# Kernel optimization log

Hardware: AMD Instinct MI355X
Metric: run time of the kernel (lower is better)

## Reference

```python
import jax, jax.numpy as jnp
import numpy as np
import math

# ---- module config (mirrors init_kwargs) ----
FRAME_H, FRAME_W = 480, 640
HFOV = 79.0
CAM_H_CM = 88.0            # camera_height * 100
NUM_SEM = 16
RES = 5                    # map_resolution (cm/cell)
MAP_SIZE_CM = 4800
DSC = 4                    # global_downscaling
DU = 4                     # du_scale
VR = 100                   # vision_range (cells)
CAT_THR, EXP_THR, MAP_THR = 5.0, 1.0, 1.0
MIN_D_CM, MAX_D_CM = 50.0, 350.0
NC = 6                     # MC.NON_SEM_CHANNELS
ML = MAP_SIZE_CM // DSC // RES   # 240 local map cells
MG = MAP_SIZE_CM // RES          # 960 global map cells
ZMIN = int(-40 / RES)            # -8
ZB = int(360 / RES) - ZMIN       # 80 z bins
MIN_MAP_H = int(25 / RES - ZMIN)            # 13
MAX_MAP_H = int((CAM_H_CM + 1) / RES - ZMIN)  # 25
BC_R = 200 // RES                # been-close radius (cells)
CENTER_POSE = (ML * RES) / 200.0 # agent start at local map center (m)


def _affine_grid(theta, H, W):
    # theta: (B,2,3); align_corners=True convention
    ys = jnp.linspace(-1.0, 1.0, H)
    xs = jnp.linspace(-1.0, 1.0, W)
    xg, yg = jnp.meshgrid(xs, ys)
    base = jnp.stack([xg, yg, jnp.ones_like(xg)], -1)  # (H,W,3)
    return jnp.einsum('bij,hwj->bhwi', theta, base)    # (B,H,W,2)


def _grid_sample(img, grid):
    # bilinear, align_corners=True, zero padding (matches F.grid_sample)
    B, C, H, W = img.shape
    x = (grid[..., 0] + 1.0) * 0.5 * (W - 1)
    y = (grid[..., 1] + 1.0) * 0.5 * (H - 1)
    x0, y0 = jnp.floor(x), jnp.floor(y)
    flat = img.reshape(B, C, H * W)
    out = jnp.zeros_like(img)
    for dx in (0.0, 1.0):
        for dy in (0.0, 1.0):
            xi, yi = x0 + dx, y0 + dy
            w = (1.0 - jnp.abs(x - xi)) * (1.0 - jnp.abs(y - yi))
            ok = (xi >= 0) & (xi <= W - 1) & (yi >= 0) & (yi <= H - 1)
            idx = (jnp.clip(yi, 0, H - 1).astype(jnp.int32) * W
                   + jnp.clip(xi, 0, W - 1).astype(jnp.int32))
            g = jnp.take_along_axis(flat, jnp.broadcast_to(idx.reshape(B, 1, -1), (B, C, H * W)), axis=2)
            out = out + g.reshape(B, C, H, W) * (w * ok)[:, None]
    return out


def _splat(gx, gy, gz, feat, valid):
    # trilinear scatter-add of per-point features into (VR,VR,ZB) voxel grid
    # gx,gy,gz,valid: (B,P); feat: (B,P,F)
    B, P = gx.shape
    F = feat.shape[-1]
    ncell = VR * VR * ZB
    acc = jnp.zeros((B * ncell, F), feat.dtype)
    base = (jnp.arange(B) * ncell)[:, None]
    x0, y0, z0 = jnp.floor(gx), jnp.floor(gy), jnp.floor(gz)
    for dx in (0.0, 1.0):
        for dy in (0.0, 1.0):
            for dz in (0.0, 1.0):
                xi, yi, zi = x0 + dx, y0 + dy, z0 + dz
                w = (1.0 - jnp.abs(gx - xi)) * (1.0 - jnp.abs(gy - yi)) * (1.0 - jnp.abs(gz - zi))
                ok = valid & (xi >= 0) & (xi < VR) & (yi >= 0) & (yi < VR) & (zi >= 0) & (zi < ZB)
                cell = (yi.astype(jnp.int32) * VR + xi.astype(jnp.int32)) * ZB + zi.astype(jnp.int32)
                idx = jnp.clip(base + cell, 0, B * ncell - 1).reshape(-1)
                upd = (feat * (w * ok.astype(feat.dtype))[..., None]).reshape(B * P, F)
                acc = acc.at[idx].add(upd)
    return acc.reshape(B, VR, VR, ZB, F).transpose(0, 4, 1, 2, 3)  # (B,F,VR,VR,ZB)


def _forward(seq_obs, seq_pose_delta, seq_camera_poses, init_local_map,
             init_global_map, init_local_pose, init_global_pose,
             init_lmb, init_origins, seq_dones, seq_update_global):
    B, T = seq_obs.shape[:2]
    C = NUM_SEM
    f = FRAME_W / (2.0 * math.tan(math.radians(HFOV) / 2.0))
    cx, cy = FRAME_W / 2.0, FRAME_H / 2.0
    xs = ((jnp.arange(0, FRAME_W, DU) - cx) / f).astype(jnp.float32)   # (Ws,)
    zr = ((cy - jnp.arange(0, FRAME_H, DU)) / f).astype(jnp.float32)   # (Hs,)
    # camera tilt (elevation) from extrinsics (identity -> 0)
    elev = jnp.arctan2(seq_camera_poses[:, 2, 1], seq_camera_poses[:, 2, 2])
    ce, se = jnp.cos(elev)[:, None, None], jnp.sin(elev)[:, None, None]
    Hs, Ws = FRAME_H // DU, FRAME_W // DU
    P = Hs * Ws
    row = jnp.arange(ML, dtype=jnp.float32)

    def step(carry, inp):
        local_map, global_map, pose = carry
        obs, pd, done, upd = inp
        done = done.astype(bool)
        upd = upd.astype(bool)
        # episode reset
        local_map = jnp.where(done[:, None, None, None], 0.0, local_map)
        global_map = jnp.where(done[:, None, None, None], 0.0, global_map)
        pose = jnp.where(done[:, None], jnp.array([CENTER_POSE, CENTER_POSE, 0.0], jnp.float32), pose)
        # pose update (get_new_pose_batch, degrees)
        tr = jnp.radians(pose[:, 2])
        nx = pose[:, 0] + pd[:, 0] * jnp.cos(tr) - pd[:, 1] * jnp.sin(tr)
        ny = pose[:, 1] + pd[:, 0] * jnp.sin(tr) + pd[:, 1] * jnp.cos(tr)
        nt = jnp.mod(pose[:, 2] + jnp.degrees(pd[:, 2]) + 180.0, 360.0) - 180.0
        pose = jnp.stack([nx, ny, nt], -1)
        # ---- depth -> egocentric point cloud (cm) ----
        d = obs[:, 3, ::DU, ::DU]                           # (B,Hs,Ws)
        valid = (d >= MIN_D_CM) & (d <= MAX_D_CM)
        lat = d * xs[None, None, :]
        up = d * zr[None, :, None]
        fwd = d * ce + up * se
        hgt = -d * se + up * ce + CAM_H_CM
        gx = (lat / RES + VR / 2.0).reshape(B, P)
        gy = (fwd / RES).reshape(B, P)
        gz = (hgt / RES - ZMIN).reshape(B, P)
        # features: occupancy + avg-pooled semantics (du_scale pooling)
        sem = obs[:, 4:].reshape(B, C, Hs, DU, Ws, DU).mean((3, 5))
        feat = jnp.concatenate([jnp.ones((B, 1, Hs, Ws), obs.dtype), sem], 1)
        feat = feat.reshape(B, 1 + C, P).transpose(0, 2, 1)  # (B,P,F)
        vox = _splat(gx, gy, gz, feat, valid.reshape(B, P))  # (B,F,VR,VR,ZB)
        agent_hp = vox[..., MIN_MAP_H:MAX_MAP_H].sum(-1)
        all_hp = vox.sum(-1)
        fp_map = jnp.clip(agent_hp[:, 0:1] / MAP_THR, 0.0, 1.0)
        fp_exp = jnp.clip(all_hp[:, 0:1] / EXP_THR, 0.0, 1.0)
        sem_pred = jnp.clip(agent_hp[:, 1:] / CAT_THR, 0.0, 1.0)
        agent_view = jnp.zeros((B, NC + C, ML, ML), obs.dtype)
        y1, x1 = ML // 2, ML // 2 - VR // 2
        agent_view = agent_view.at[:, 0:1, y1:y1 + VR, x1:x1 + VR].set(fp_map)
        agent_view = agent_view.at[:, 1:2, y1:y1 + VR, x1:x1 + VR].set(fp_exp)
        agent_view = agent_view.at[:, NC:, y1:y1 + VR, x1:x1 + VR].set(sem_pred)
        # ---- pose transform: rotation then translation grid_sample ----
        th = jnp.radians(90.0 - pose[:, 2])
        stx = -(pose[:, 0] * 100.0 / RES - ML / 2.0) / (ML / 2.0)
        sty = -(pose[:, 1] * 100.0 / RES - ML / 2.0) / (ML / 2.0)
        c, s = jnp.cos(th), jnp.sin(th)
        z0 = jnp.zeros_like(th)
        o1 = jnp.ones_like(th)
        th_rot = jnp.stack([jnp.stack([c, -s, z0], -1), jnp.stack([s, c, z0], -1)], 1)
        th_tr = jnp.stack([jnp.stack([o1, z0, stx], -1), jnp.stack([z0, o1, sty], -1)], 1)
        warped = _grid_sample(_grid_sample(agent_view, _affine_grid(th_rot, ML, ML)),
                              _affine_grid(th_tr, ML, ML))
        # dilate obstacle channel (3x3 ones kernel, 1 iter)
        obst = jax.lax.reduce_window(warped[:, 0:1], -jnp.inf, jax.lax.max,
                                     (1, 1, 3, 3), (1, 1, 1, 1), 'SAME')
        warped = warped.at[:, 0:1].set(obst)
        local_map = jnp.maximum(local_map, warped)
        # current location / visited / been-close disks
        acx, acy = pose[:, 0] * 100.0 / RES, pose[:, 1] * 100.0 / RES
        d2 = ((row[None, None, :] - acx[:, None, None]) ** 2
              + (row[None, :, None] - acy[:, None, None]) ** 2)
        curr = (d2 <= 4.0).astype(local_map.dtype)
        local_map = local_map.at[:, 2].set(curr)
        local_map = local_map.at[:, 3].max(curr)
        local_map = local_map.at[:, 4].max((d2 <= float(BC_R ** 2)).astype(local_map.dtype))
        # global map update at local map boundaries
        gnew = jax.vmap(lambda g, l, lm: jax.lax.dynamic_update_slice(g, l, (0, lm[0], lm[2])))(
            global_map, local_map, init_lmb)
        global_map = jnp.where(upd[:, None, None, None], gnew, global_map)
        gpose = pose + init_origins
        # map features: local NC ch + maxpooled global NC ch + local sem ch
        gmax = global_map[:, :NC].reshape(B, NC, MG // DSC, DSC, MG // DSC, DSC).max((3, 5))
        mf = jnp.concatenate([local_map[:, :NC], gmax, local_map[:, NC:]], 1)
        return (local_map, global_map, pose), (mf, pose, gpose)

    xs_t = (jnp.swapaxes(seq_obs, 0, 1), jnp.swapaxes(seq_pose_delta, 0, 1),
            jnp.swapaxes(seq_dones, 0, 1), jnp.swapaxes(seq_update_global, 0, 1))
    (fl, fg, _), (mfs, lps, gps) = jax.lax.scan(
        step, (init_local_map, init_global_map, init_local_pose), xs_t)
    seq_mf = jnp.swapaxes(mfs, 0, 1)
    seq_lp = jnp.swapaxes(lps, 0, 1)
    seq_gp = jnp.swapaxes(gps, 0, 1)
    seq_lmb = jnp.broadcast_to(init_lmb[:, None], (B, T, 4))
    seq_org = jnp.broadcast_to(init_origins[:, None], (B, T, 3))
    return seq_mf, fl, fg, seq_lp, seq_gp, seq_lmb, seq_org


def setup_inputs():
    key = jax.random.key(0)
    k0, k1 = jax.random.split(key)
    B, T = 4, 4
    obs = jax.random.uniform(k0, (B, T, 4 + NUM_SEM, FRAME_H, FRAME_W), jnp.float32)
    obs = obs.at[:, :, 3].set(MIN_D_CM + obs[:, :, 3] * (MAX_D_CM - MIN_D_CM))  # depth in cm
    obs = obs.at[:, :, 4:].set((obs[:, :, 4:] > 0.9).astype(jnp.float32))       # binary seg masks
    pd = jax.random.normal(k1, (B, T, 3), jnp.float32) * jnp.array([0.25, 0.05, 0.1], jnp.float32)
    lo = (MG - ML) // 2
    lmb = jnp.tile(jnp.array([[lo, lo + ML, lo, lo + ML]], jnp.int32), (B, 1))
    origins = jnp.concatenate([jnp.full((B, 2), lo * RES / 100.0, jnp.float32),
                               jnp.zeros((B, 1), jnp.float32)], 1)
    lp = jnp.concatenate([jnp.full((B, 2), CENTER_POSE, jnp.float32),
                          jnp.zeros((B, 1), jnp.float32)], 1)
    return {
        "seq_obs": obs,
        "seq_pose_delta": pd,
        "seq_camera_poses": jnp.broadcast_to(jnp.eye(4, dtype=jnp.float32), (B, 4, 4)),
        "init_local_map": jnp.zeros((B, NC + NUM_SEM, ML, ML), jnp.float32),
        "init_global_map": jnp.zeros((B, NC + NUM_SEM, MG, MG), jnp.float32),
        "init_local_pose": lp,
        "init_global_pose": lp + origins,
        "init_origins": origins,
        "seq_dones": jnp.zeros((B, T), jnp.int32),
        "seq_update_global": jnp.ones((B, T), jnp.int32),
        "init_lmb": lmb,
    }


def reference(seq_obs, seq_pose_delta, seq_camera_poses, init_local_map, init_global_map,
              init_local_pose, init_global_pose, init_origins, seq_dones,
              seq_update_global, init_lmb):
    return _forward(seq_obs, seq_pose_delta, seq_camera_poses, init_local_map,
                    init_global_map, init_local_pose, init_global_pose,
                    init_lmb, init_origins, seq_dones, seq_update_global)
```

## Files before the change

### kernel.cpp

```cpp
#include <hip/hip_runtime.h>
#include <math.h>

#ifndef M_PI
#define M_PI 3.14159265358979323846
#endif

#define BB 4
#define TT 4
#define NSEM 16
#define CHL 22
#define CHMF 28
#define ML 240
#define MG 960
#define VR 100
#define HS 120
#define WSW 160
#define NPL 18
#define CPAD 24
#define MLSQ (ML*ML)
#define MGSQ (MG*MG)
#define VRSQ (VR*VR)
#define PPT (HS*WSW)
#define NPART 12
#define PR 9
#define NGRP 5

#define SZ_MF (BB*TT*CHMF*MLSQ)
#define SZ_FL (BB*CHL*MLSQ)
#define SZ_FG (BB*CHL*MGSQ)
#define OFF_FL SZ_MF
#define OFF_FG (OFF_FL + SZ_FL)
#define OFF_LP (OFF_FG + SZ_FG)
#define OFF_GP (OFF_LP + BB*TT*3)
#define OFF_LMB (OFF_GP + BB*TT*3)
#define OFF_ORG (OFF_LMB + BB*TT*4)

#define WS_SCAL 0
#define WS_FLAGS (WS_SCAL + BB*TT*8)
#define WS_CACHE (WS_FLAGS + 4*BB)
#define WS_PLANES (WS_CACHE + BB*6*MLSQ)
#define WS_I2 (WS_PLANES + BB*TT*VRSQ*CPAD)
#define PTSN (BB*TT*PPT)
#define WS_GY (WS_I2 + BB*TT*NPL*MLSQ)
#define WS_GX (WS_GY + PTSN)
#define WS_WZA (WS_GX + PTSN)
#define WS_WZL (WS_WZA + PTSN)
#define WS_SEMDS (WS_WZL + PTSN)

__global__ __launch_bounds__(256) void k_stage1(const float* __restrict__ obs,
                                                const float* __restrict__ cam,
                                                const float* __restrict__ pd,
                                                const float* __restrict__ ilp,
                                                const float* __restrict__ org,
                                                const int* __restrict__ lmb,
                                                const int* __restrict__ dones,
                                                const int* __restrict__ updg,
                                                float* __restrict__ out,
                                                float* __restrict__ ws)
{
    if (blockIdx.x == 0) {
        int i = threadIdx.x;
        if (i < BB*TT) {
            int b = i / TT, t = i % TT;
            for (int k = 0; k < 4; k++) out[OFF_LMB + (b*TT+t)*4 + k] = (float)lmb[b*4+k];
            for (int k = 0; k < 3; k++) out[OFF_ORG + (b*TT+t)*3 + k] = org[b*3+k];
        }
        if (i >= BB) return;
        int b = i;
        float p0 = ilp[b*3+0], p1 = ilp[b*3+1], p2 = ilp[b*3+2];
        const float D2R = 0.017453292519943295f;
        int lastDone = -1, lastUpd = -1;
        for (int t = 0; t < TT; t++) {
            if (dones[b*TT+t]) { p0 = 6.0f; p1 = 6.0f; p2 = 0.0f; lastDone = t; }
            if (updg[b*TT+t]) lastUpd = t;
            float tr = p2 * D2R;
            float c0 = cosf(tr), s0 = sinf(tr);
            float q0 = pd[(b*TT+t)*3+0], q1 = pd[(b*TT+t)*3+1], q2 = pd[(b*TT+t)*3+2];
            float nx = p0 + q0*c0 - q1*s0;
            float ny = p1 + q0*s0 + q1*c0;
            float a  = p2 + q2*57.29577951308232f + 180.0f;
            float m  = fmodf(a, 360.0f); if (m < 0.0f) m += 360.0f;
            float nt = m - 180.0f;
            p0 = nx; p1 = ny; p2 = nt;
            out[OFF_LP + (b*TT+t)*3+0] = nx;
            out[OFF_LP + (b*TT+t)*3+1] = ny;
            out[OFF_LP + (b*TT+t)*3+2] = nt;
            out[OFF_GP + (b*TT+t)*3+0] = nx + org[b*3+0];
            out[OFF_GP + (b*TT+t)*3+1] = ny + org[b*3+1];
            out[OFF_GP + (b*TT+t)*3+2] = nt + org[b*3+2];
            float th = (90.0f - nt) * D2R;
            float ax = nx*100.0f/5.0f, ay = ny*100.0f/5.0f;
            float* sc = ws + WS_SCAL + (b*TT+t)*8;
            sc[0] = cosf(th);
            sc[1] = sinf(th);
            sc[2] = -(ax - 120.0f)/120.0f;
            sc[3] = -(ay - 120.0f)/120.0f;
            sc[4] = ax;
            sc[5] = ay;
        }
        ws[WS_FLAGS + b*4 + 0] = (lastDone >= 0) ? 1.0f : 0.0f;
        ws[WS_FLAGS + b*4 + 1] = (lastUpd < lastDone) ? 1.0f : 0.0f;
        ws[WS_FLAGS + b*4 + 2] = (float)lastUpd;
        return;
    }
    int bb = blockIdx.x - 1;
    int bt = bb / 75;
    int b = bt / TT;
    int p = (bb % 75)*256 + threadIdx.x;
    int h = p / WSW, w = p % WSW;
    size_t pi = (size_t)bt*PPT + p;
    const float* ob = obs + (size_t)bt * 20 * 480 * 640;
    float d = ob[(size_t)(3*480 + 4*h)*640 + 4*w];
    if (!(d >= 50.0f && d <= 350.0f)) { ws[WS_GY + pi] = -1000.0f; return; }

    double fd = 640.0 / (2.0 * tan((79.0 * M_PI / 180.0) * 0.5));
    float ff  = (float)fd;
    float xsv = (float)(4*w - 320) / ff;
    float zrv = (240.0f - (float)(4*h)) / ff;
    float elev = atan2f(cam[b*16+9], cam[b*16+10]);
    float ce = cosf(elev), se = sinf(elev);
    float up  = d * zrv;
    float fwd = d*ce + up*se;
    float hgt = -d*se + up*ce + 88.0f;
    float gx = (d*xsv)/5.0f + 50.0f;
    float gy = fwd/5.0f;
    float gz = hgt/5.0f + 8.0f;

    float z0 = floorf(gz);
    float wza = 0.0f, wzl = 0.0f;
    #pragma unroll
    for (int dz = 0; dz < 2; dz++) {
        float zi = z0 + dz;
        float wz = 1.0f - fabsf(gz - zi);
        if (zi >= 0.0f && zi < 80.0f) {
            wzl += wz;
            if (zi >= 13.0f && zi < 25.0f) wza += wz;
        }
    }
    if (wzl == 0.0f && wza == 0.0f) { ws[WS_GY + pi] = -1000.0f; return; }

    ws[WS_GY + pi]  = gy;
    ws[WS_GX + pi]  = gx;
    ws[WS_WZA + pi] = wza;
    ws[WS_WZL + pi] = wzl;

    if (wza > 0.0f) {
        const float* sb = ob + (size_t)4*480*640 + (size_t)(4*h)*640 + 4*w;
        float* so = ws + WS_SEMDS + (size_t)bt*NSEM*PPT + p;
        #pragma unroll
        for (int k = 0; k < NSEM; k++) {
            float s = 0.0f;
            #pragma unroll
            for (int r = 0; r < 4; r++) {
                const float4 v = *(const float4*)(sb + (size_t)k*480*640 + r*640);
                s += v.x + v.y + v.z + v.w;
            }
            so[(size_t)k*PPT] = s * 0.0625f;
        }
    }
}

__global__ __launch_bounds__(256) void k_splat2(const float* __restrict__ ws,
                                                float* __restrict__ planes)
{
    int bt = blockIdx.x;
    int part = blockIdx.y;
    int grp = blockIdx.z;
    int rlo = part * PR;
    int c0  = (grp == 0) ? 0 : (2 + 4*(grp-1));
    int nch = (grp == 0) ? 2 : 4;
    __shared__ float acc[4*PR*VR];
    for (int e = threadIdx.x; e < nch*PR*VR; e += 256) acc[e] = 0.0f;
    __syncthreads();

    const float* gyA  = ws + WS_GY  + (size_t)bt*PPT;
    const float* gxA  = ws + WS_GX  + (size_t)bt*PPT;
    const float* wzaA = ws + WS_WZA + (size_t)bt*PPT;
    const float* wzlA = ws + WS_WZL + (size_t)bt*PPT;
    const float* semA = ws + WS_SEMDS + (size_t)bt*NSEM*PPT + (size_t)(c0-2)*PPT;

    for (int p = threadIdx.x; p < PPT; p += 256) {
        float gy = gyA[p];
        float y0 = floorf(gy);
        if (y0 > (float)(rlo + PR - 1) || y0 + 1.0f < (float)rlo) continue;
        float wza = wzaA[p];
        if (grp != 0 && wza <= 0.0f) continue;
        float gx  = gxA[p];
        float x0 = floorf(gx);
        float sem[4];
        if (grp != 0) {
            #pragma unroll
            for (int k = 0; k < 4; k++) sem[k] = semA[(size_t)k*PPT + p];
        }
        float wzl = (grp == 0) ? wzlA[p] : 0.0f;
        #pragma unroll
        for (int dy = 0; dy < 2; dy++) {
            float yi = y0 + dy;
            if (!(yi >= 0.0f && yi < 100.0f)) continue;
            int r = (int)yi - rlo;
            if (r < 0 || r >= PR) continue;
            float wy = 1.0f - fabsf(gy - yi);
            #pragma unroll
            for (int dx = 0; dx < 2; dx++) {
                float xi = x0 + dx;
                if (!(xi >= 0.0f && xi < 100.0f)) continue;
                float wxy = (1.0f - fabsf(gx - xi)) * wy;
                if (wxy <= 0.0f) continue;
                int cell = r*VR + (int)xi;
                if (grp == 0) {
                    if (wza > 0.0f) atomicAdd(&acc[cell], wza*wxy);
                    if (wzl > 0.0f) atomicAdd(&acc[PR*VR + cell], wzl*wxy);
                } else {
                    #pragma unroll
                    for (int k = 0; k < 4; k++) {
                        float sv = sem[k];
                        if (sv != 0.0f) atomicAdd(&acc[k*PR*VR + cell], sv*wza*wxy);
                    }
                }
            }
        }
    }
    __syncthreads();

    int nrows = 100 - rlo; if (nrows > PR) nrows = PR;
    if (nrows <= 0) return;
    float* pl = planes + (size_t)bt*VRSQ*CPAD;
    for (int e = threadIdx.x; e < nch*nrows*VR; e += 256) {
        int c = e / (nrows*VR);
        int rc = e % (nrows*VR);
        int r = rc / VR, x = rc % VR;
        pl[(size_t)((rlo + r)*VR + x)*CPAD + (c0 + c)] = acc[c*PR*VR + r*VR + x];
    }
}

__global__ __launch_bounds__(256) void k_stage3(const float* __restrict__ planes,
                                                const float* __restrict__ igm,
                                                const int* __restrict__ dones,
                                                const int* __restrict__ lmb,
                                                float* __restrict__ I2,
                                                float* __restrict__ fg,
                                                float* __restrict__ out,
                                                float* __restrict__ ws)
{
    int bid = blockIdx.x;
    if (bid < 3600) {
        int bt = bid / 225;
        int idx = (bid % 225)*256 + threadIdx.x;
        int i = idx / ML, j = idx % ML;
        const float* sc = ws + WS_SCAL + bt*8;
        float c = sc[0], s = sc[1], stx = sc[2], sty = sc[3];
        float* o = I2 + (size_t)bt*NPL*MLSQ + idx;
        const float* pl = planes + (size_t)bt*VRSQ*CPAD;

        int   soff[16];
        float sw[16];
        float wsum = 0.0f;
        {
            float xg = (float)j * (float)(2.0/239.0) - 1.0f + stx;
            float yg = (float)i * (float)(2.0/239.0) - 1.0f + sty;
            float x = (xg + 1.0f)*0.5f*239.0f;
            float y = (yg + 1.0f)*0.5f*239.0f;
            float x0 = floorf(x), y0 = floorf(y);
            #pragma unroll
            for (int dy = 0; dy < 2; dy++) {
                float yi = y0 + dy;
                bool vy = (yi >= 0.0f && yi <= 239.0f);
                float wy = 1.0f - fabsf(y - yi);
                #pragma unroll
                for (int dx = 0; dx < 2; dx++) {
                    float xi = x0 + dx;
                    bool vx = (xi >= 0.0f && xi <= 239.0f);
                    float w2v = (vy && vx) ? (1.0f - fabsf(x - xi)) * wy : 0.0f;
                    int ci = (dy*2 + dx)*4;
                    float xg1 = (float)(int)xi * (float)(2.0/239.0) - 1.0f;
                    float yg1 = (float)(int)yi * (float)(2.0/239.0) - 1.0f;
                    float gxr = c*xg1 - s*yg1;
                    float gyr = s*xg1 + c*yg1;
                    float xx = (gxr + 1.0f)*0.5f*239.0f;
                    float yy = (gyr + 1.0f)*0.5f*239.0f;
                    float xx0 = floorf(xx), yy0 = floorf(yy);
                    #pragma unroll
                    for (int dy1 = 0; dy1 < 2; dy1++) {
                        float syi = yy0 + dy1;
                        bool v1y = (syi >= 120.0f && syi < 220.0f);
                        float wy1 = 1.0f - fabsf(yy - syi);
                        #pragma unroll
                        for (int dx1 = 0; dx1 < 2; dx1++) {
                            float sxi = xx0 + dx1;
                            bool v1 = v1y && (sxi >= 70.0f && sxi < 170.0f);
                            float w1v = v1 ? (1.0f - fabsf(xx - sxi)) * wy1 : 0.0f;
                            float wt = w2v * w1v;
                            soff[ci + dy1*2 + dx1] = v1 ? ((int)syi - 120)*VR + ((int)sxi - 70) : 0;
                            sw[ci + dy1*2 + dx1] = wt;
                            wsum += wt;
                        }
                    }
                }
            }
        }

        if (wsum <= 0.0f) {
            #pragma unroll
            for (int cc = 0; cc < NPL; cc++) o[(size_t)cc*MLSQ] = 0.0f;
            return;
        }
        float acc[NPL];
        #pragma unroll
        for (int cc = 0; cc < NPL; cc++) acc[cc] = 0.0f;
        #pragma unroll
        for (int k = 0; k < 16; k++) {
            float w = sw[k];
            if (w == 0.0f) continue;
            const float* pb = pl + (size_t)soff[k]*CPAD;
            float4 a0 = *(const float4*)(pb + 0);
            float4 a1 = *(const float4*)(pb + 4);
            float4 a2 = *(const float4*)(pb + 8);
            float4 a3 = *(const float4*)(pb + 12);
            float2 a4 = *(const float2*)(pb + 16);
            acc[0]  += fminf(a0.x, 1.0f) * w;
            acc[1]  += fminf(a0.y, 1.0f) * w;
            acc[2]  += fminf(a0.z / 5.0f, 1.0f) * w;
            acc[3]  += fminf(a0.w / 5.0f, 1.0f) * w;
            acc[4]  += fminf(a1.x / 5.0f, 1.0f) * w;
            acc[5]  += fminf(a1.y / 5.0f, 1.0f) * w;
            acc[6]  += fminf(a1.z / 5.0f, 1.0f) * w;
            acc[7]  += fminf(a1.w / 5.0f, 1.0f) * w;
            acc[8]  += fminf(a2.x / 5.0f, 1.0f) * w;
            acc[9]  += fminf(a2.y / 5.0f, 1.0f) * w;
            acc[10] += fminf(a2.z / 5.0f, 1.0f) * w;
            acc[11] += fminf(a2.w / 5.0f, 1.0f) * w;
            acc[12] += fminf(a3.x / 5.0f, 1.0f) * w;
            acc[13] += fminf(a3.y / 5.0f, 1.0f) * w;
            acc[14] += fminf(a3.z / 5.0f, 1.0f) * w;
            acc[15] += fminf(a3.w / 5.0f, 1.0f) * w;
            acc[16] += fminf(a4.x / 5.0f, 1.0f) * w;
            acc[17] += fminf(a4.y / 5.0f, 1.0f) * w;
        }
        #pragma unroll
        for (int cc = 0; cc < NPL; cc++) o[(size_t)cc*MLSQ] = acc[cc];
        return;
    }
    int fb = bid - 3600;
    int blk = fb % 225;
    int c = (fb / 225) % CHL;
    int b = fb / (225*CHL);
    int idx = blk*256 + threadIdx.x;
    int i = idx / ML, j = idx % ML;
    bool anyDone = ws[WS_FLAGS + b*4 + 0] > 0.5f;
    bool zeroWin = ws[WS_FLAGS + b*4 + 1] > 0.5f;
    int lastUpd  = (int)ws[WS_FLAGS + b*4 + 2];
    int y0 = lmb[b*4+0], x0 = lmb[b*4+2];
    int iy0 = y0 >> 2, ix0 = x0 >> 2;
    bool inWin = (i >= iy0) && (i < iy0 + ML/4) && (j >= ix0) && (j < ix0 + ML/4);

    size_t base = ((size_t)b*CHL + c)*MGSQ + (size_t)(4*i)*MG + 4*j;
    const float* g = igm + base;
    float* go = fg + base;

    int act;
    if (inWin) act = zeroWin ? 1 : ((lastUpd >= 0) ? 2 : (anyDone ? 1 : 0));
    else       act = anyDone ? 1 : 0;

    if (c < 6) {
        float m = -3.0e38f;
        #pragma unroll
        for (int r = 0; r < 4; r++) {
            float4 q = *(const float4*)(g + (size_t)r*MG);
            if (act == 0) *(float4*)(go + (size_t)r*MG) = q;
            else if (act == 1) *(float4*)(go + (size_t)r*MG) = make_float4(0,0,0,0);
            m = fmaxf(m, fmaxf(fmaxf(q.x, q.y), fmaxf(q.z, q.w)));
        }
        ws[WS_CACHE + ((size_t)b*6 + c)*MLSQ + idx] = m;
        if (!inWin) {
            float v = m;
            for (int t = 0; t < TT; t++) {
                if (dones[b*TT+t]) v = 0.0f;
                out[(size_t)(b*TT+t)*CHMF*MLSQ + (6+c)*MLSQ + idx] = v;
            }
        }
    } else {
        if (act == 2) return;
        if (act == 1) {
            float4 z = make_float4(0,0,0,0);
            #pragma unroll
            for (int r = 0; r < 4; r++) *(float4*)(go + (size_t)r*MG) = z;
        } else {
            #pragma unroll
            for (int r = 0; r < 4; r++)
                *(float4*)(go + (size_t)r*MG) = *(const float4*)(g + (size_t)r*MG);
        }
    }
}

__global__ __launch_bounds__(256) void k_updl7(const float* __restrict__ I2,
                                               const float* __restrict__ ws,
                                               const float* __restrict__ ilm,
                                               const int* __restrict__ dones,
                                               const int* __restrict__ updg,
                                               const int* __restrict__ lmb,
                                               float* __restrict__ fl,
                                               float* __restrict__ fg,
                                               float* __restrict__ out)
{
    int bz = blockIdx.z;
    int b = bz / 7, g = bz % 7;
    int gi = blockIdx.y;
    int bx = blockIdx.x;
    int lane = threadIdx.x & 63, wv = threadIdx.x >> 6;
    int j0 = (bx < 3) ? bx*64 : 176;
    int j = j0 + lane;
    int i = gi*4 + wv;
    int idx = i*ML + j;

    int ncl, cl[4];
    switch (g) {
        case 0:  ncl = 1; cl[0] = 0; cl[1] = 0; cl[2] = 0; cl[3] = 0; break;
        case 1:  ncl = 3; cl[0] = 1; cl[1] = 2; cl[2] = 3; cl[3] = 0; break;
        case 2:  ncl = 2; cl[0] = 4; cl[1] = 5; cl[2] = 0; cl[3] = 0; break;
        default: ncl = 4; { int cc0 = 6 + (g-3)*4;
                 cl[0] = cc0; cl[1] = cc0+1; cl[2] = cc0+2; cl[3] = cc0+3; } break;
    }
    bool hasG = (g <= 2);

    __shared__ float red[4][3][16];

    const float* lmsrc = ilm + (size_t)b*CHL*MLSQ;
    float* lm = fl + (size_t)b*CHL*MLSQ;
    int y0 = lmb[b*4+0], x0 = lmb[b*4+2];
    bool zeroWin = ws[WS_FLAGS + b*4 + 1] > 0.5f;
    int lastUpd = (int)ws[WS_FLAGS + b*4 + 2];

    float S[4];
    #pragma unroll
    for (int q = 0; q < 4; q++) {
        int c = cl[q];
        S[q] = (q < ncl && c != 2) ? lmsrc[c*MLSQ + idx] : 0.0f;
    }

    bool writer = hasG && (wv == 0) && ((lane & 3) == 0);
    int cx = lane >> 2;
    int cellY = (y0 >> 2) + gi;
    int cellX = (x0 >> 2) + (j0 >> 2) + cx;
    float W[3];
    if (writer) {
        #pragma unroll
        for (int q = 0; q < 3; q++)
            if (q < ncl)
                W[q] = ws[WS_CACHE + ((size_t)b*6 + cl[q])*MLSQ + cellY*ML + cellX];
    }

    for (int t = 0; t < TT; t++) {
        int bt = b*TT + t;
        bool done = dones[bt] != 0;
        bool upd  = updg[bt] != 0;
        const float* src = I2 + (size_t)bt*NPL*MLSQ;
        float* mf = out + (size_t)bt*CHMF*MLSQ;

        float pooled = -3.0e38f;
        if (g == 0) {
            for (int di = -1; di <= 1; di++) {
                int ii = i + di; if (ii < 0 || ii >= ML) continue;
                for (int dj = -1; dj <= 1; dj++) {
                    int jj = j + dj; if (jj < 0 || jj >= ML) continue;
                    pooled = fmaxf(pooled, src[ii*ML + jj]);
                }
            }
        }
        const float* sc = ws + WS_SCAL + bt*8;
        float acx = sc[4], acy = sc[5];
        float ddx = (float)j - acx, ddy = (float)i - acy;
        float d2 = ddx*ddx + ddy*ddy;
        float curr = (d2 <= 4.0f) ? 1.0f : 0.0f;
        float bc   = (d2 <= 1600.0f) ? 1.0f : 0.0f;

        size_t goff = (size_t)(y0+i)*MG + (x0+j);
        bool wrG = (t == lastUpd) && !zeroWin;

        #pragma unroll
        for (int q = 0; q < 4; q++) {
            if (q >= ncl) continue;
            int c = cl[q];
            if (done) S[q] = 0.0f;
            float nv;
            if      (c == 0) nv = fmaxf(S[q], pooled);
            else if (c == 1) nv = fmaxf(S[q], src[MLSQ + idx]);
            else if (c == 2) nv = curr;
            else if (c == 3) nv = fmaxf(S[q], curr);
            else if (c == 4) nv = fmaxf(S[q], bc);
            else if (c == 5) nv = S[q];
            else             nv = fmaxf(S[q], src[(size_t)(c-4)*MLSQ + idx]);
            S[q] = nv;
            mf[(size_t)(c < 6 ? c : c + 6)*MLSQ + idx] = nv;
            if (wrG) fg[((size_t)b*CHL + c)*MGSQ + goff] = nv;
        }

        if (hasG) {
            #pragma unroll
            for (int q = 0; q < 3; q++) {
                if (q >= ncl) continue;
                float v = S[q];
                v = fmaxf(v, __shfl_xor(v, 1, 64));
                v = fmaxf(v, __shfl_xor(v, 2, 64));
                if ((lane & 3) == 0) red[wv][q][cx] = v;
            }
            __syncthreads();
            if (writer) {
                #pragma unroll
                for (int q = 0; q < 3; q++) {
                    if (q >= ncl) continue;
                    if (done) W[q] = 0.0f;
                    if (upd)  W[q] = fmaxf(fmaxf(red[0][q][cx], red[1][q][cx]),
                                           fmaxf(red[2][q][cx], red[3][q][cx]));
                    mf[(size_t)(6 + cl[q])*MLSQ + cellY*ML + cellX] = W[q];
                }
            }
            __syncthreads();
        }
    }
    #pragma unroll
    for (int q = 0; q < 4; q++)
        if (q < ncl) lm[(size_t)cl[q]*MLSQ + idx] = S[q];
}

extern "C" void kernel_launch(void* const* d_in, const int* in_sizes, int n_in,
                              void* d_out, int out_size, void* d_ws, size_t ws_size,
                              hipStream_t stream)
{
    const float* obs   = (const float*)d_in[0];
    const float* pd    = (const float*)d_in[1];
    const float* cam   = (const float*)d_in[2];
    const float* ilm   = (const float*)d_in[3];
    const float* igm   = (const float*)d_in[4];
    const float* ilp   = (const float*)d_in[5];
    const float* org   = (const float*)d_in[7];
    const int*   dones = (const int*)d_in[8];
    const int*   updg  = (const int*)d_in[9];
    const int*   lmb   = (const int*)d_in[10];
    float* out = (float*)d_out;
    float* ws  = (float*)d_ws;

    float* fl     = out + OFF_FL;
    float* fg     = out + OFF_FG;
    float* planes = ws + WS_PLANES;
    float* I2v    = ws + WS_I2;

    k_stage1<<<1 + 75*BB*TT, 256, 0, stream>>>(obs, cam, pd, ilp, org, lmb,
                                               dones, updg, out, ws);
    k_splat2<<<dim3(BB*TT, NPART, NGRP), 256, 0, stream>>>(ws, planes);
    k_stage3<<<3600 + 225*CHL*BB, 256, 0, stream>>>(planes, igm, dones, lmb,
                                                    I2v, fg, out, ws);
    k_updl7<<<dim3(4, 60, BB*7), 256, 0, stream>>>(I2v, ws, ilm, dones, updg, lmb,
                                                   fl, fg, out);
}
```

Measured before the change: 358.4 us.

## Bound grid-sample and pooling work by rotated-window bounding box; fuse splat with global-map copy

Stage 1 now computes, per (batch,time), an axis-aligned bounding box of where the rotated and translated 100x100 egocentric window can land in the 240x240 local map. The grid-sample becomes its own 16x16-tiled kernel that skips tiles outside that box. The local-map update skips max-pooling and I2 reads outside the box and substitutes zero. The splat work is merged into the same launch as the global-map copy blocks so they overlap. The risk is that the skipped tiles are never written in I2, so correctness depends on the box plus margin fully covering every nonzero sample.

```diff
diff --git a/kernel.cpp b/kernel.cpp
--- a/kernel.cpp
+++ b/kernel.cpp
@@ -24,6 +24,7 @@
 #define NPART 12
 #define PR 9
 #define NGRP 5
+#define NSPLAT (BB*TT*NPART*NGRP)
 
 #define SZ_MF (BB*TT*CHMF*MLSQ)
 #define SZ_FL (BB*CHL*MLSQ)
@@ -37,7 +38,8 @@
 
 #define WS_SCAL 0
 #define WS_FLAGS (WS_SCAL + BB*TT*8)
-#define WS_CACHE (WS_FLAGS + 4*BB)
+#define WS_AABB (WS_FLAGS + 4*BB)
+#define WS_CACHE (WS_AABB + 4*BB*TT)
 #define WS_PLANES (WS_CACHE + BB*6*MLSQ)
 #define WS_I2 (WS_PLANES + BB*TT*VRSQ*CPAD)
 #define PTSN (BB*TT*PPT)
@@ -90,13 +92,33 @@
             out[OFF_GP + (b*TT+t)*3+2] = nt + org[b*3+2];
             float th = (90.0f - nt) * D2R;
             float ax = nx*100.0f/5.0f, ay = ny*100.0f/5.0f;
+            float cth = cosf(th), sth = sinf(th);
+            float stxv = -(ax - 120.0f)/120.0f;
+            float styv = -(ay - 120.0f)/120.0f;
             float* sc = ws + WS_SCAL + (b*TT+t)*8;
-            sc[0] = cosf(th);
-            sc[1] = sinf(th);
-            sc[2] = -(ax - 120.0f)/120.0f;
-            sc[3] = -(ay - 120.0f)/120.0f;
+            sc[0] = cth;
+            sc[1] = sth;
+            sc[2] = stxv;
+            sc[3] = styv;
             sc[4] = ax;
             sc[5] = ay;
+            float imin = 1e9f, imax = -1e9f, jmin = 1e9f, jmax = -1e9f;
+            #pragma unroll
+            for (int q = 0; q < 4; q++) {
+                float cx = (q & 1) ? 170.0f : 69.0f;
+                float cy = (q & 2) ? 220.0f : 119.0f;
+                float dj =  cth*(cx - 119.5f) + sth*(cy - 119.5f);
+                float di = -sth*(cx - 119.5f) + cth*(cy - 119.5f);
+                float jv = 119.5f + dj - stxv*119.5f;
+                float iv = 119.5f + di - styv*119.5f;
+                imin = fminf(imin, iv); imax = fmaxf(imax, iv);
+                jmin = fminf(jmin, jv); jmax = fmaxf(jmax, jv);
+            }
+            float* ab = ws + WS_AABB + (b*TT+t)*4;
+            ab[0] = floorf(imin) - 3.0f;
+            ab[1] = ceilf(imax) + 3.0f;
+            ab[2] = floorf(jmin) - 3.0f;
+            ab[3] = ceilf(jmax) + 3.0f;
         }
         ws[WS_FLAGS + b*4 + 0] = (lastDone >= 0) ? 1.0f : 0.0f;
         ws[WS_FLAGS + b*4 + 1] = (lastUpd < lastDone) ? 1.0f : 0.0f;
@@ -160,187 +182,87 @@
     }
 }
 
-__global__ __launch_bounds__(256) void k_splat2(const float* __restrict__ ws,
-                                                float* __restrict__ planes)
-{
-    int bt = blockIdx.x;
-    int part = blockIdx.y;
-    int grp = blockIdx.z;
-    int rlo = part * PR;
-    int c0  = (grp == 0) ? 0 : (2 + 4*(grp-1));
-    int nch = (grp == 0) ? 2 : 4;
-    __shared__ float acc[4*PR*VR];
-    for (int e = threadIdx.x; e < nch*PR*VR; e += 256) acc[e] = 0.0f;
-    __syncthreads();
-
-    const float* gyA  = ws + WS_GY  + (size_t)bt*PPT;
-    const float* gxA  = ws + WS_GX  + (size_t)bt*PPT;
-    const float* wzaA = ws + WS_WZA + (size_t)bt*PPT;
-    const float* wzlA = ws + WS_WZL + (size_t)bt*PPT;
-    const float* semA = ws + WS_SEMDS + (size_t)bt*NSEM*PPT + (size_t)(c0-2)*PPT;
-
-    for (int p = threadIdx.x; p < PPT; p += 256) {
-        float gy = gyA[p];
-        float y0 = floorf(gy);
-        if (y0 > (float)(rlo + PR - 1) || y0 + 1.0f < (float)rlo) continue;
-        float wza = wzaA[p];
-        if (grp != 0 && wza <= 0.0f) continue;
-        float gx  = gxA[p];
-        float x0 = floorf(gx);
-        float sem[4];
-        if (grp != 0) {
-            #pragma unroll
-            for (int k = 0; k < 4; k++) sem[k] = semA[(size_t)k*PPT + p];
-        }
-        float wzl = (grp == 0) ? wzlA[p] : 0.0f;
-        #pragma unroll
-        for (int dy = 0; dy < 2; dy++) {
-            float yi = y0 + dy;
-            if (!(yi >= 0.0f && yi < 100.0f)) continue;
-            int r = (int)yi - rlo;
-            if (r < 0 || r >= PR) continue;
-            float wy = 1.0f - fabsf(gy - yi);
-            #pragma unroll
-            for (int dx = 0; dx < 2; dx++) {
-                float xi = x0 + dx;
-                if (!(xi >= 0.0f && xi < 100.0f)) continue;
-                float wxy = (1.0f - fabsf(gx - xi)) * wy;
-                if (wxy <= 0.0f) continue;
-                int cell = r*VR + (int)xi;
-                if (grp == 0) {
-                    if (wza > 0.0f) atomicAdd(&acc[cell], wza*wxy);
-                    if (wzl > 0.0f) atomicAdd(&acc[PR*VR + cell], wzl*wxy);
-                } else {
-                    #pragma unroll
-                    for (int k = 0; k < 4; k++) {
-                        float sv = sem[k];
-                        if (sv != 0.0f) atomicAdd(&acc[k*PR*VR + cell], sv*wza*wxy);
-                    }
-                }
-            }
-        }
-    }
-    __syncthreads();
-
-    int nrows = 100 - rlo; if (nrows > PR) nrows = PR;
-    if (nrows <= 0) return;
-    float* pl = planes + (size_t)bt*VRSQ*CPAD;
-    for (int e = threadIdx.x; e < nch*nrows*VR; e += 256) {
-        int c = e / (nrows*VR);
-        int rc = e % (nrows*VR);
-        int r = rc / VR, x = rc % VR;
-        pl[(size_t)((rlo + r)*VR + x)*CPAD + (c0 + c)] = acc[c*PR*VR + r*VR + x];
-    }
-}
-
-__global__ __launch_bounds__(256) void k_stage3(const float* __restrict__ planes,
-                                                const float* __restrict__ igm,
+__global__ __launch_bounds__(256) void k_stage2(const float* __restrict__ igm,
                                                 const int* __restrict__ dones,
                                                 const int* __restrict__ lmb,
-                                                float* __restrict__ I2,
+                                                float* __restrict__ planes,
                                                 float* __restrict__ fg,
                                                 float* __restrict__ out,
                                                 float* __restrict__ ws)
 {
+    __shared__ float acc[4*PR*VR];
     int bid = blockIdx.x;
-    if (bid < 3600) {
-        int bt = bid / 225;
-        int idx = (bid % 225)*256 + threadIdx.x;
-        int i = idx / ML, j = idx % ML;
-        const float* sc = ws + WS_SCAL + bt*8;
-        float c = sc[0], s = sc[1], stx = sc[2], sty = sc[3];
-        float* o = I2 + (size_t)bt*NPL*MLSQ + idx;
-        const float* pl = planes + (size_t)bt*VRSQ*CPAD;
-
-        int   soff[16];
-        float sw[16];
-        float wsum = 0.0f;
-        {
-            float xg = (float)j * (float)(2.0/239.0) - 1.0f + stx;
-            float yg = (float)i * (float)(2.0/239.0) - 1.0f + sty;
-            float x = (xg + 1.0f)*0.5f*239.0f;
-            float y = (yg + 1.0f)*0.5f*239.0f;
-            float x0 = floorf(x), y0 = floorf(y);
+    if (bid < NSPLAT) {
+        int bt = bid & 15;
+        int part = (bid >> 4) % NPART;
+        int grp = bid / (16*NPART);
+        int rlo = part * PR;
+        int c0  = (grp == 0) ? 0 : (2 + 4*(grp-1));
+        int nch = (grp == 0) ? 2 : 4;
+        for (int e = threadIdx.x; e < nch*PR*VR; e += 256) acc[e] = 0.0f;
+        __syncthreads();
+
+        const float* gyA  = ws + WS_GY  + (size_t)bt*PPT;
+        const float* gxA  = ws + WS_GX  + (size_t)bt*PPT;
+        const float* wzaA = ws + WS_WZA + (size_t)bt*PPT;
+        const float* wzlA = ws + WS_WZL + (size_t)bt*PPT;
+        const float* semA = ws + WS_SEMDS + (size_t)bt*NSEM*PPT + (size_t)(c0-2)*PPT;
+
+        for (int p = threadIdx.x; p < PPT; p += 256) {
+            float gy = gyA[p];
+            float y0 = floorf(gy);
+            if (y0 > (float)(rlo + PR - 1) || y0 + 1.0f < (float)rlo) continue;
+            float wza = wzaA[p];
+            if (grp != 0 && wza <= 0.0f) continue;
+            float gx  = gxA[p];
+            float x0 = floorf(gx);
+            float sem[4];
+            if (grp != 0) {
+                #pragma unroll
+                for (int k = 0; k < 4; k++) sem[k] = semA[(size_t)k*PPT + p];
+            }
+            float wzl = (grp == 0) ? wzlA[p] : 0.0f;
             #pragma unroll
             for (int dy = 0; dy < 2; dy++) {
                 float yi = y0 + dy;
-                bool vy = (yi >= 0.0f && yi <= 239.0f);
-                float wy = 1.0f - fabsf(y - yi);
+                if (!(yi >= 0.0f && yi < 100.0f)) continue;
+                int r = (int)yi - rlo;
+                if (r < 0 || r >= PR) continue;
+                float wy = 1.0f - fabsf(gy - yi);
                 #pragma unroll
                 for (int dx = 0; dx < 2; dx++) {
                     float xi = x0 + dx;
-                    bool vx = (xi >= 0.0f && xi <= 239.0f);
-                    float w2v = (vy && vx) ? (1.0f - fabsf(x - xi)) * wy : 0.0f;
-                    int ci = (dy*2 + dx)*4;
-                    float xg1 = (float)(int)xi * (float)(2.0/239.0) - 1.0f;
-                    float yg1 = (float)(int)yi * (float)(2.0/239.0) - 1.0f;
-                    float gxr = c*xg1 - s*yg1;
-                    float gyr = s*xg1 + c*yg1;
-                    float xx = (gxr + 1.0f)*0.5f*239.0f;
-                    float yy = (gyr + 1.0f)*0.5f*239.0f;
-                    float xx0 = floorf(xx), yy0 = floorf(yy);
-                    #pragma unroll
-                    for (int dy1 = 0; dy1 < 2; dy1++) {
-                        float syi = yy0 + dy1;
-                        bool v1y = (syi >= 120.0f && syi < 220.0f);
-                        float wy1 = 1.0f - fabsf(yy - syi);
+                    if (!(xi >= 0.0f && xi < 100.0f)) continue;
+                    float wxy = (1.0f - fabsf(gx - xi)) * wy;
+                    if (wxy <= 0.0f) continue;
+                    int cell = r*VR + (int)xi;
+                    if (grp == 0) {
+                        if (wza > 0.0f) atomicAdd(&acc[cell], wza*wxy);
+                        if (wzl > 0.0f) atomicAdd(&acc[PR*VR + cell], wzl*wxy);
+                    } else {
                         #pragma unroll
-                        for (int dx1 = 0; dx1 < 2; dx1++) {
-                            float sxi = xx0 + dx1;
-                            bool v1 = v1y && (sxi >= 70.0f && sxi < 170.0f);
-                            float w1v = v1 ? (1.0f - fabsf(xx - sxi)) * wy1 : 0.0f;
-                            float wt = w2v * w1v;
-                            soff[ci + dy1*2 + dx1] = v1 ? ((int)syi - 120)*VR + ((int)sxi - 70) : 0;
-                            sw[ci + dy1*2 + dx1] = wt;
-                            wsum += wt;
+                        for (int k = 0; k < 4; k++) {
+                            float sv = sem[k];
+                            if (sv != 0.0f) atomicAdd(&acc[k*PR*VR + cell], sv*wza*wxy);
                         }
                     }
                 }
             }
         }
-
-        if (wsum <= 0.0f) {
-            #pragma unroll
-            for (int cc = 0; cc < NPL; cc++) o[(size_t)cc*MLSQ] = 0.0f;
-            return;
-        }
-        float acc[NPL];
-        #pragma unroll
-        for (int cc = 0; cc < NPL; cc++) acc[cc] = 0.0f;
-        #pragma unroll
-        for (int k = 0; k < 16; k++) {
-            float w = sw[k];
-            if (w == 0.0f) continue;
-            const float* pb = pl + (size_t)soff[k]*CPAD;
-            float4 a0 = *(const float4*)(pb + 0);
-            float4 a1 = *(const float4*)(pb + 4);
-            float4 a2 = *(const float4*)(pb + 8);
-            float4 a3 = *(const float4*)(pb + 12);
-            float2 a4 = *(const float2*)(pb + 16);
-            acc[0]  += fminf(a0.x, 1.0f) * w;
-            acc[1]  += fminf(a0.y, 1.0f) * w;
-            acc[2]  += fminf(a0.z / 5.0f, 1.0f) * w;
-            acc[3]  += fminf(a0.w / 5.0f, 1.0f) * w;
-            acc[4]  += fminf(a1.x / 5.0f, 1.0f) * w;
-            acc[5]  += fminf(a1.y / 5.0f, 1.0f) * w;
-            acc[6]  += fminf(a1.z / 5.0f, 1.0f) * w;
-            acc[7]  += fminf(a1.w / 5.0f, 1.0f) * w;
-            acc[8]  += fminf(a2.x / 5.0f, 1.0f) * w;
-            acc[9]  += fminf(a2.y / 5.0f, 1.0f) * w;
-            acc[10] += fminf(a2.z / 5.0f, 1.0f) * w;
-            acc[11] += fminf(a2.w / 5.0f, 1.0f) * w;
-            acc[12] += fminf(a3.x / 5.0f, 1.0f) * w;
-            acc[13] += fminf(a3.y / 5.0f, 1.0f) * w;
-            acc[14] += fminf(a3.z / 5.0f, 1.0f) * w;
-            acc[15] += fminf(a3.w / 5.0f, 1.0f) * w;
-            acc[16] += fminf(a4.x / 5.0f, 1.0f) * w;
-            acc[17] += fminf(a4.y / 5.0f, 1.0f) * w;
-        }
-        #pragma unroll
-        for (int cc = 0; cc < NPL; cc++) o[(size_t)cc*MLSQ] = acc[cc];
+        __syncthreads();
+
+        int nrows = 100 - rlo; if (nrows > PR) nrows = PR;
+        if (nrows <= 0) return;
+        float* pl = planes + (size_t)bt*VRSQ*CPAD;
+        for (int e = threadIdx.x; e < nch*nrows*VR; e += 256) {
+            int c = e / (nrows*VR);
+            int rc = e % (nrows*VR);
+            int r = rc / VR, x = rc % VR;
+            pl[(size_t)((rlo + r)*VR + x)*CPAD + (c0 + c)] = acc[c*PR*VR + r*VR + x];
+        }
         return;
     }
-    int fb = bid - 3600;
+    int fb = bid - NSPLAT;
     int blk = fb % 225;
     int c = (fb / 225) % CHL;
     int b = fb / (225*CHL);
@@ -390,6 +312,112 @@
                 *(float4*)(go + (size_t)r*MG) = *(const float4*)(g + (size_t)r*MG);
         }
     }
+}
+
+__global__ __launch_bounds__(256) void k_gs(const float* __restrict__ planes,
+                                            const float* __restrict__ ws,
+                                            float* __restrict__ I2)
+{
+    int bt = blockIdx.z;
+    const float* ab = ws + WS_AABB + bt*4;
+    int ilo = (int)ab[0], ihi = (int)ab[1], jlo = (int)ab[2], jhi = (int)ab[3];
+    int r0 = blockIdx.y*16, q0 = blockIdx.x*16;
+    if (r0+15 < ilo-2 || r0 > ihi+2 || q0+15 < jlo-2 || q0 > jhi+2) return;
+
+    int i = r0 + (threadIdx.x >> 4);
+    int j = q0 + (threadIdx.x & 15);
+    int idx = i*ML + j;
+    const float* sc = ws + WS_SCAL + bt*8;
+    float c = sc[0], s = sc[1], stx = sc[2], sty = sc[3];
+    float* o = I2 + (size_t)bt*NPL*MLSQ + idx;
+    const float* pl = planes + (size_t)bt*VRSQ*CPAD;
+
+    int   soff[16];
+    float sw[16];
+    float wsum = 0.0f;
+    {
+        float xg = (float)j * (float)(2.0/239.0) - 1.0f + stx;
+        float yg = (float)i * (float)(2.0/239.0) - 1.0f + sty;
+        float x = (xg + 1.0f)*0.5f*239.0f;
+        float y = (yg + 1.0f)*0.5f*239.0f;
+        float x0 = floorf(x), y0 = floorf(y);
+        #pragma unroll
+        for (int dy = 0; dy < 2; dy++) {
+            float yi = y0 + dy;
+            bool vy = (yi >= 0.0f && yi <= 239.0f);
+            float wy = 1.0f - fabsf(y - yi);
+            #pragma unroll
+            for (int dx = 0; dx < 2; dx++) {
+                float xi = x0 + dx;
+                bool vx = (xi >= 0.0f && xi <= 239.0f);
+                float w2v = (vy && vx) ? (1.0f - fabsf(x - xi)) * wy : 0.0f;
+                int ci = (dy*2 + dx)*4;
+                float xg1 = (float)(int)xi * (float)(2.0/239.0) - 1.0f;
+                float yg1 = (float)(int)yi * (float)(2.0/239.0) - 1.0f;
+                float gxr = c*xg1 - s*yg1;
+                float gyr = s*xg1 + c*yg1;
+                float xx = (gxr + 1.0f)*0.5f*239.0f;
+                float yy = (gyr + 1.0f)*0.5f*239.0f;
+                float xx0 = floorf(xx), yy0 = floorf(yy);
+                #pragma unroll
+                for (int dy1 = 0; dy1 < 2; dy1++) {
+                    float syi = yy0 + dy1;
+                    bool v1y = (syi >= 120.0f && syi < 220.0f);
+                    float wy1 = 1.0f - fabsf(yy - syi);
+                    #pragma unroll
+                    for (int dx1 = 0; dx1 < 2; dx1++) {
+                        float sxi = xx0 + dx1;
+                        bool v1 = v1y && (sxi >= 70.0f && sxi < 170.0f);
+                        float w1v = v1 ? (1.0f - fabsf(xx - sxi)) * wy1 : 0.0f;
+                        float wt = w2v * w1v;
+                        soff[ci + dy1*2 + dx1] = v1 ? ((int)syi - 120)*VR + ((int)sxi - 70) : 0;
+                        sw[ci + dy1*2 + dx1] = wt;
+                        wsum += wt;
+                    }
+                }
+            }
+        }
+    }
+
+    if (wsum <= 0.0f) {
+        #pragma unroll
+        for (int cc = 0; cc < NPL; cc++) o[(size_t)cc*MLSQ] = 0.0f;
+        return;
+    }
+    float acc[NPL];
+    #pragma unroll
+    for (int cc = 0; cc < NPL; cc++) acc[cc] = 0.0f;
+    #pragma unroll
+    for (int k = 0; k < 16; k++) {
+        float w = sw[k];
+        if (w == 0.0f) continue;
+        const float* pb = pl + (size_t)soff[k]*CPAD;
+        float4 a0 = *(const float4*)(pb + 0);
+        float4 a1 = *(const float4*)(pb + 4);
+        float4 a2 = *(const float4*)(pb + 8);
+        float4 a3 = *(const float4*)(pb + 12);
+        float2 a4 = *(const float2*)(pb + 16);
+        acc[0]  += fminf(a0.x, 1.0f) * w;
+        acc[1]  += fminf(a0.y, 1.0f) * w;
+        acc[2]  += fminf(a0.z / 5.0f, 1.0f) * w;
+        acc[3]  += fminf(a0.w / 5.0f, 1.0f) * w;
+        acc[4]  += fminf(a1.x / 5.0f, 1.0f) * w;
+        acc[5]  += fminf(a1.y / 5.0f, 1.0f) * w;
+        acc[6]  += fminf(a1.z / 5.0f, 1.0f) * w;
+        acc[7]  += fminf(a1.w / 5.0f, 1.0f) * w;
+        acc[8]  += fminf(a2.x / 5.0f, 1.0f) * w;
+        acc[9]  += fminf(a2.y / 5.0f, 1.0f) * w;
+        acc[10] += fminf(a2.z / 5.0f, 1.0f) * w;
+        acc[11] += fminf(a2.w / 5.0f, 1.0f) * w;
+        acc[12] += fminf(a3.x / 5.0f, 1.0f) * w;
+        acc[13] += fminf(a3.y / 5.0f, 1.0f) * w;
+        acc[14] += fminf(a3.z / 5.0f, 1.0f) * w;
+        acc[15] += fminf(a3.w / 5.0f, 1.0f) * w;
+        acc[16] += fminf(a4.x / 5.0f, 1.0f) * w;
+        acc[17] += fminf(a4.y / 5.0f, 1.0f) * w;
+    }
+    #pragma unroll
+    for (int cc = 0; cc < NPL; cc++) o[(size_t)cc*MLSQ] = acc[cc];
 }
 
 __global__ __launch_bounds__(256) void k_updl7(const float* __restrict__ I2,
@@ -455,14 +483,21 @@
         bool upd  = updg[bt] != 0;
         const float* src = I2 + (size_t)bt*NPL*MLSQ;
         float* mf = out + (size_t)bt*CHMF*MLSQ;
-
-        float pooled = -3.0e38f;
+        const float* ab = ws + WS_AABB + bt*4;
+        int ilo = (int)ab[0], ihi = (int)ab[1], jlo = (int)ab[2], jhi = (int)ab[3];
+        bool inA = (i >= ilo) && (i <= ihi) && (j >= jlo) && (j <= jhi);
+
+        float pooled = 0.0f;
         if (g == 0) {
-            for (int di = -1; di <= 1; di++) {
-                int ii = i + di; if (ii < 0 || ii >= ML) continue;
-                for (int dj = -1; dj <= 1; dj++) {
-                    int jj = j + dj; if (jj < 0 || jj >= ML) continue;
-                    pooled = fmaxf(pooled, src[ii*ML + jj]);
+            bool inP = (i >= ilo-1) && (i <= ihi+1) && (j >= jlo-1) && (j <= jhi+1);
+            if (inP) {
+                pooled = -3.0e38f;
+                for (int di = -1; di <= 1; di++) {
+                    int ii = i + di; if (ii < 0 || ii >= ML) continue;
+                    for (int dj = -1; dj <= 1; dj++) {
+                        int jj = j + dj; if (jj < 0 || jj >= ML) continue;
+                        pooled = fmaxf(pooled, src[ii*ML + jj]);
+                    }
                 }
             }
         }
@@ -483,12 +518,12 @@
             if (done) S[q] = 0.0f;
             float nv;
             if      (c == 0) nv = fmaxf(S[q], pooled);
-            else if (c == 1) nv = fmaxf(S[q], src[MLSQ + idx]);
+            else if (c == 1) nv = fmaxf(S[q], inA ? src[MLSQ + idx] : 0.0f);
             else if (c == 2) nv = curr;
             else if (c == 3) nv = fmaxf(S[q], curr);
             else if (c == 4) nv = fmaxf(S[q], bc);
             else if (c == 5) nv = S[q];
-            else             nv = fmaxf(S[q], src[(size_t)(c-4)*MLSQ + idx]);
+            else             nv = fmaxf(S[q], inA ? src[(size_t)(c-4)*MLSQ + idx] : 0.0f);
             S[q] = nv;
             mf[(size_t)(c < 6 ? c : c + 6)*MLSQ + idx] = nv;
             if (wrG) fg[((size_t)b*CHL + c)*MGSQ + goff] = nv;
@@ -546,9 +581,9 @@
 
     k_stage1<<<1 + 75*BB*TT, 256, 0, stream>>>(obs, cam, pd, ilp, org, lmb,
                                                dones, updg, out, ws);
-    k_splat2<<<dim3(BB*TT, NPART, NGRP), 256, 0, stream>>>(ws, planes);
-    k_stage3<<<3600 + 225*CHL*BB, 256, 0, stream>>>(planes, igm, dones, lmb,
-                                                    I2v, fg, out, ws);
+    k_stage2<<<NSPLAT + 225*CHL*BB, 256, 0, stream>>>(igm, dones, lmb,
+                                                      planes, fg, out, ws);
+    k_gs<<<dim3(15, 15, BB*TT), 256, 0, stream>>>(planes, ws, I2v);
     k_updl7<<<dim3(4, 60, BB*7), 256, 0, stream>>>(I2v, ws, ilm, dones, updg, lmb,
                                                    fl, fg, out);
 }
```

New measurement: 336.9 us. 1.06x faster.
